# Optimization experiments

Hardware: AMD Instinct MI355X
Metric: run time of the kernel (lower is better)

Reference implementation:

```python
import jax, jax.numpy as jnp
import numpy as np

EPS = 1e-10
WS = 5  # window_size
PAD = WS // 2


def _conv(x, k, pad_h, pad_w):
    # x: [N,1,H,W], k: [1,1,kh,kw], 'same'-style explicit padding
    return jax.lax.conv_general_dilated(
        x, k, window_strides=(1, 1),
        padding=[(pad_h, pad_h), (pad_w, pad_w)],
        dimension_numbers=("NCHW", "OIHW", "NCHW"))


def setup_inputs() -> dict:
    key = jax.random.key(0)
    B, C, Fr, T = 8, 2, 256, 2048
    spectrogram = jax.random.normal(key, (B, C, Fr, T), dtype=jnp.float32)
    # Gaussian kernel (window_size=5, sigma=1.0)
    c = WS // 2
    coords = jnp.arange(WS, dtype=jnp.float32) - c
    yy, xx = jnp.meshgrid(coords, coords, indexing="ij")
    g = jnp.exp(-(xx ** 2 + yy ** 2) / 2.0)
    gaussian_kernel = (g / g.sum()).reshape(1, 1, WS, WS)
    # Sobel kernels / 8
    sobel_x = (jnp.array([[-1, 0, 1], [-2, 0, 2], [-1, 0, 1]], jnp.float32) / 8.0).reshape(1, 1, 3, 3)
    sobel_y = (jnp.array([[-1, -2, -1], [0, 0, 0], [1, 2, 1]], jnp.float32) / 8.0).reshape(1, 1, 3, 3)
    # Harmonic kernel: 7x1 [-1,0,0,2,0,0,-1]
    hk = jnp.zeros(7, jnp.float32).at[0].set(-1.0).at[3].set(2.0).at[6].set(-1.0)
    harmonic_kernel = hk.reshape(1, 1, 7, 1)
    return {"spectrogram": spectrogram, "gaussian_kernel": gaussian_kernel,
            "sobel_x": sobel_x, "sobel_y": sobel_y, "harmonic_kernel": harmonic_kernel}


def _forward(spectrogram, gaussian_kernel, sobel_x, sobel_y, harmonic_kernel):
    B, C, Fr, T = spectrogram.shape
    # Per-channel 1-in/1-out convs == fold channels into batch.
    x = spectrogram.reshape(B * C, 1, Fr, T)

    grad_freq = _conv(x, sobel_y, 1, 1)
    grad_time = _conv(x, sobel_x, 1, 1)
    magnitude = jnp.sqrt(grad_freq ** 2 + grad_time ** 2 + EPS)
    angle = jnp.arctan2(grad_freq, grad_time + EPS)

    # ---- entropy (structure-tensor eigenvalue entropy) ----
    vx = magnitude * jnp.cos(angle)
    vy = magnitude * jnp.sin(angle)
    vxx = _conv(vx * vx, gaussian_kernel, PAD, PAD)
    vyy = _conv(vy * vy, gaussian_kernel, PAD, PAD)
    vxy = _conv(vx * vy, gaussian_kernel, PAD, PAD)
    trace = vxx + vyy
    det = vxx * vyy - vxy * vxy
    disc = jnp.sqrt(jnp.maximum(trace * trace - 4.0 * det, 0.0) + EPS)
    l1 = jnp.maximum((trace + disc) / 2.0, EPS)
    l2 = jnp.maximum((trace - disc) / 2.0, EPS)
    s = l1 + l2 + EPS
    p1, p2 = l1 / s, l2 / s
    entropy = -(p1 * jnp.log(p1 + EPS) + p2 * jnp.log(p2 + EPS)) / np.log(2.0)
    entropy = jnp.clip(entropy, 0.0, 1.0)

    # ---- alignment ----
    ux = jnp.cos(angle)
    uy = jnp.sin(angle)
    ux_avg = _conv(ux, gaussian_kernel, PAD, PAD)
    uy_avg = _conv(uy, gaussian_kernel, PAD, PAD)
    alignment = jnp.clip(jnp.sqrt(ux_avg ** 2 + uy_avg ** 2 + EPS), 0.0, 1.0)

    # ---- curvature ----
    dudx = _conv(ux, sobel_x, 1, 1)
    dudy = _conv(ux, sobel_y, 1, 1)
    dvdx = _conv(uy, sobel_x, 1, 1)
    dvdy = _conv(uy, sobel_y, 1, 1)
    curv = jnp.sqrt(dudx ** 2 + dudy ** 2 + dvdx ** 2 + dvdy ** 2 + EPS)
    curvature = _conv(curv, gaussian_kernel, PAD, PAD)

    # ---- harmonic coherence ----
    harm = jnp.abs(_conv(x, harmonic_kernel, 3, 0))
    local_energy = _conv(x ** 2, gaussian_kernel, PAD, PAD)
    harmonic = jnp.clip(harm / (local_energy + EPS), 0.0, 1.0)

    # ---- temporal stability: inverse temporal gradient magnitude, smoothed ----
    temporal = _conv(1.0 / (1.0 + jnp.abs(grad_time)), gaussian_kernel, PAD, PAD)
    temporal = jnp.clip(temporal, 0.0, 1.0)

    # ---- spectral flow: smoothed frequency-gradient magnitude ----
    spectral = jnp.clip(_conv(jnp.abs(grad_freq), gaussian_kernel, PAD, PAD), 0.0, 1.0)

    def chan_mean(f):  # [B*C,1,F,T] -> [B,1,F,T]
        return f.reshape(B, C, Fr, T).mean(axis=1, keepdims=True)

    return (chan_mean(entropy), chan_mean(alignment), chan_mean(curvature),
            chan_mean(harmonic), chan_mean(temporal), chan_mean(spectral))


def reference(spectrogram, gaussian_kernel, sobel_x, sobel_y, harmonic_kernel):
    return _forward(spectrogram, gaussian_kernel, sobel_x, sobel_y, harmonic_kernel)
```

## Files before the change

kernel.cpp:

```cpp
#include <hip/hip_runtime.h>
#include <hip/hip_fp16.h>


#define F_DIM 256
#define T_DIM 2048
#define B_DIM 8
#define C_DIM 2
#define TILE  32

#define XROWS 40
#define XS    42
#define UROWS 38
#define US    38
#define FROWS 36
#define FS    36
#define FH2   18
#define EPSF  1e-10f

static __device__ __forceinline__ __half2 pack_h2(float a, float b) {
    auto v = __builtin_amdgcn_cvt_pkrtz(a, b);
    return *(__half2*)&v;
}
static __device__ __forceinline__ float clamp01(float x) {
    return fminf(fmaxf(x, 0.f), 1.f);
}

__global__ __launch_bounds__(256, 4)
void audio_struct_fused(const float* __restrict__ x_in,
                        const float* __restrict__ gk_in,
                        float* __restrict__ out)
{
    __shared__ __align__(16) float   s_x [XROWS*XS];
    __shared__ __align__(16) __half2 s_u [UROWS*US];
    __shared__ __align__(16) __half2 s_P0[FROWS*FS];
    __shared__ __align__(16) __half2 s_P1[FROWS*FS];
    __shared__ __align__(16) __half2 s_P2[FROWS*FS];
    __shared__ __align__(16) float   s_tmp[TILE*FS];

    const int tx  = threadIdx.x;
    const int ty  = threadIdx.y;
    const int tid = ty * 32 + tx;
    const int t0  = blockIdx.x * TILE;
    const int f0  = blockIdx.y * TILE;
    const int b   = blockIdx.z;

    float r0 = gk_in[10], r1 = gk_in[11], r2 = gk_in[12], r3 = gk_in[13], r4 = gk_in[14];
    float winv = __builtin_amdgcn_rcpf(r0 + r1 + r2 + r3 + r4);
    const float w[5] = {r0*winv, r1*winv, r2*winv, r3*winv, r4*winv};
    const __half2 wh2[5] = {pack_h2(w[0],w[0]), pack_h2(w[1],w[1]), pack_h2(w[2],w[2]),
                            pack_h2(w[3],w[3]), pack_h2(w[4],w[4])};

    auto vpass_pair = [&](const __half2* src, __half2* dst) {
        const uint2* s = (const uint2*)src;
        uint2* d = (uint2*)dst;
        for (int idx = tid; idx < TILE * FH2; idx += 256) {
            __half2 a0 = pack_h2(0.f, 0.f), a1 = a0;
            #pragma unroll
            for (int i = 0; i < 5; ++i) {
                uint2 v = s[idx + i * FH2];
                a0 = __hfma2(wh2[i], *(const __half2*)&v.x, a0);
                a1 = __hfma2(wh2[i], *(const __half2*)&v.y, a1);
            }
            uint2 o; o.x = *(const unsigned*)&a0; o.y = *(const unsigned*)&a1;
            d[idx] = o;
        }
    };

    float acc[6][4];
    #pragma unroll
    for (int k = 0; k < 6; ++k)
        #pragma unroll
        for (int s = 0; s < 4; ++s) acc[k][s] = 0.0f;

    for (int c = 0; c < C_DIM; ++c) {
        __syncthreads();

        const float* xp = x_in + (size_t)(b * C_DIM + c) * F_DIM * T_DIM;
        for (int idx = tid; idx < XROWS * 20; idx += 256) {
            int r  = idx / 20, c2 = idx % 20;
            int gf = f0 + r - 4;
            int gt = t0 + c2 * 2 - 4;
            float2 v = make_float2(0.f, 0.f);
            if ((unsigned)gf < (unsigned)F_DIM && (unsigned)gt < (unsigned)T_DIM)
                v = *(const float2*)(xp + (size_t)gf * T_DIM + gt);
            *(float2*)&s_x[r * XS + c2 * 2] = v;
        }
        __syncthreads();

        for (int idx = tid; idx < UROWS * UROWS; idx += 256) {
            int r = idx / UROWS, cc = idx % UROWS;
            int gfr = f0 + r - 3, gtc = t0 + cc - 3;
            float ux = 0.f, uy = 0.f, trp = 0.f, dfp = 0.f, sxy = 0.f,
                  tin = 0.f, sf = 0.f;
            if ((unsigned)gfr < (unsigned)F_DIM && (unsigned)gtc < (unsigned)T_DIM) {
                const float* xc = &s_x[(r + 1) * XS + (cc + 1)];
                float x00 = xc[-XS-1], x01 = xc[-XS], x02 = xc[-XS+1];
                float x10 = xc[-1],                   x12 = xc[1];
                float x20 = xc[XS-1],  x21 = xc[XS],  x22 = xc[XS+1];
                float gfv = ((x20 + 2.f*x21 + x22) - (x00 + 2.f*x01 + x02)) * 0.125f;
                float gtv = ((x02 + 2.f*x12 + x22) - (x00 + 2.f*x10 + x20)) * 0.125f;
                float gte = gtv + EPSF;
                float rh  = __builtin_amdgcn_rsqf(gfv * gfv + gte * gte);
                ux = gte * rh;
                uy = gfv * rh;
                float mag = __builtin_amdgcn_sqrtf(gfv * gfv + gtv * gtv + EPSF);
                float vx = mag * ux, vy = mag * uy;
                trp = vx * vx + vy * vy;
                dfp = (vx - vy) * (vx + vy);
                sxy = vx * vy;
                tin = __builtin_amdgcn_rcpf(1.0f + fabsf(gtv));
                sf  = fabsf(gfv);
            }
            s_u[r * US + cc] = pack_h2(ux, uy);
            if (r >= 1 && r < UROWS - 1 && cc >= 1 && cc < UROWS - 1) {
                int fi = (r - 1) * FS + (cc - 1);
                s_P0[fi] = pack_h2(trp, dfp);
                s_P1[fi] = pack_h2(sxy, tin);
                s_P2[fi] = pack_h2(sf, 0.f);
            }
        }
        __syncthreads();

        for (int idx = tid; idx < FROWS * FROWS; idx += 256) {
            int r = idx / FROWS, cc = idx % FROWS;
            int gfr = f0 + r - 2, gtc = t0 + cc - 2;
            float cv = 0.0f;
            if ((unsigned)gfr < (unsigned)F_DIM && (unsigned)gtc < (unsigned)T_DIM) {
                const __half2* up = &s_u[r * US + cc];
                float2 u00 = __half22float2(up[0]),      u01 = __half22float2(up[1]),       u02 = __half22float2(up[2]);
                float2 u10 = __half22float2(up[US]),                                        u12 = __half22float2(up[US+2]);
                float2 u20 = __half22float2(up[2*US]),   u21 = __half22float2(up[2*US+1]),  u22 = __half22float2(up[2*US+2]);
                float dudx = ((u02.x + 2.f*u12.x + u22.x) - (u00.x + 2.f*u10.x + u20.x)) * 0.125f;
                float dudy = ((u20.x + 2.f*u21.x + u22.x) - (u00.x + 2.f*u01.x + u02.x)) * 0.125f;
                float dvdx = ((u02.y + 2.f*u12.y + u22.y) - (u00.y + 2.f*u10.y + u20.y)) * 0.125f;
                float dvdy = ((u20.y + 2.f*u21.y + u22.y) - (u00.y + 2.f*u01.y + u02.y)) * 0.125f;
                cv = __builtin_amdgcn_sqrtf(dudx*dudx + dudy*dudy + dvdx*dvdx + dvdy*dvdy + EPSF);
            }
            ((__half*)s_P2)[2 * (r * FS + cc) + 1] = __float2half_rn(cv);
        }
        __syncthreads();

        float trace_s[4], diff_s[4];
        __half2* tmp_h2 = (__half2*)s_tmp;

        vpass_pair(s_P0, tmp_h2);
        __syncthreads();

        #pragma unroll
        for (int s = 0; s < 4; ++s) {
            int ry = ty + 8 * s;
            float a = 0.f, bv = 0.f;
            #pragma unroll
            for (int j = 0; j < 5; ++j) {
                float2 v = __half22float2(tmp_h2[ry * FS + tx + j]);
                a += w[j] * v.x; bv += w[j] * v.y;
            }
            trace_s[s] = a; diff_s[s] = bv;
        }
        vpass_pair(s_P1, s_P0);
        __syncthreads();

        #pragma unroll
        for (int s = 0; s < 4; ++s) {
            int ry = ty + 8 * s;
            __half2 a = pack_h2(0.f, 0.f);
            #pragma unroll
            for (int j = 0; j < 5; ++j)
                a = __hfma2(wh2[j], s_P0[ry * FS + tx + j], a);
            float2 v = __half22float2(a);
            float trace = trace_s[s], diff = diff_s[s];
            float disc  = __builtin_amdgcn_sqrtf(
                              fmaxf(diff * diff + 4.f * v.x * v.x, 0.f) + EPSF);
            float l1 = fmaxf(0.5f * (trace + disc), EPSF);
            float l2 = fmaxf(0.5f * (trace - disc), EPSF);
            float inv = __builtin_amdgcn_rcpf(l1 + l2 + EPSF);
            float p1 = l1 * inv, p2 = l2 * inv;
            float ent = -(p1 * __builtin_amdgcn_logf(p1 + EPSF)
                        + p2 * __builtin_amdgcn_logf(p2 + EPSF));
            acc[0][s] += 0.5f * clamp01(ent);
            acc[4][s] += 0.5f * clamp01(v.y);
        }
        vpass_pair(s_P2, tmp_h2);
        __syncthreads();

        #pragma unroll
        for (int s = 0; s < 4; ++s) {
            int ry = ty + 8 * s;
            __half2 a = pack_h2(0.f, 0.f);
            #pragma unroll
            for (int j = 0; j < 5; ++j)
                a = __hfma2(wh2[j], tmp_h2[ry * FS + tx + j], a);
            float2 v = __half22float2(a);
            acc[5][s] += 0.5f * clamp01(v.x);
            acc[2][s] += 0.5f * v.y;
        }
        for (int idx = tid; idx < TILE * FS; idx += 256) {
            int r = idx / FS, cc = idx % FS;
            __half2 a = pack_h2(0.f, 0.f);
            #pragma unroll
            for (int i = 0; i < 5; ++i)
                a = __hfma2(wh2[i], s_u[(r + i + 1) * US + (cc + 1)], a);
            s_P1[idx] = a;
        }
        __syncthreads();

        #pragma unroll
        for (int s = 0; s < 4; ++s) {
            int ry = ty + 8 * s;
            __half2 a = pack_h2(0.f, 0.f);
            #pragma unroll
            for (int j = 0; j < 5; ++j)
                a = __hfma2(wh2[j], s_P1[ry * FS + tx + j], a);
            float2 v = __half22float2(a);
            acc[1][s] += 0.5f * clamp01(
                __builtin_amdgcn_sqrtf(v.x * v.x + v.y * v.y + EPSF));
        }
        for (int idx = tid; idx < TILE * FS; idx += 256) {
            int r = idx / FS, cc = idx % FS;
            float a = 0.f;
            #pragma unroll
            for (int i = 0; i < 5; ++i) {
                float xv = s_x[(r + i + 2) * XS + (cc + 2)];
                a += w[i] * xv * xv;
            }
            s_tmp[idx] = a;
        }
        __syncthreads();

        #pragma unroll
        for (int s = 0; s < 4; ++s) {
            int ry = ty + 8 * s;
            float le = 0.f;
            #pragma unroll
            for (int j = 0; j < 5; ++j)
                le += w[j] * s_tmp[ry * FS + tx + j];
            float xm  = s_x[(ry + 1) * XS + tx + 4];
            float x0v = s_x[(ry + 4) * XS + tx + 4];
            float xpv = s_x[(ry + 7) * XS + tx + 4];
            float harm = fabsf(2.f * x0v - xm - xpv);
            acc[3][s] += 0.5f * clamp01(harm * __builtin_amdgcn_rcpf(le + EPSF));
        }
    }

    const size_t plane = (size_t)B_DIM * F_DIM * T_DIM;
    const size_t base  = (size_t)b * F_DIM * T_DIM + (size_t)f0 * T_DIM + t0 + tx;
    #pragma unroll
    for (int k = 0; k < 6; ++k)
        #pragma unroll
        for (int s = 0; s < 4; ++s)
            out[k * plane + base + (size_t)(ty + 8 * s) * T_DIM] = acc[k][s];
}

extern "C" void kernel_launch(void* const* d_in, const int* in_sizes, int n_in,
                              void* d_out, int out_size, void* d_ws, size_t ws_size,
                              hipStream_t stream) {
    const float* x  = (const float*)d_in[0];
    const float* gk = (const float*)d_in[1];
    float* out = (float*)d_out;
    dim3 grid(T_DIM / TILE, F_DIM / TILE, B_DIM);
    dim3 block(32, 8);
    audio_struct_fused<<<grid, block, 0, stream>>>(x, gk, out);
}
```

Before: 225.2 us.

## Use persistent blocks with atomic tile queue and register prefetch of next input

Replaces the one-block-per-tile grid with a fixed set of persistent blocks that take tiles from a global atomic counter. Each block prefetches the next channel's or next tile's input halo into registers while computing the current one, so global loads overlap with compute. It also merges a few LDS phases to drop some barriers, computes the curvature Sobel in packed half2, and reuses buffers. The costs are a second small launch to zero the counter, more register pressure from the prefetch buffer, and some lost fp32 precision in curvature.

```diff
diff --git a/kernel.cpp b/kernel.cpp
--- a/kernel.cpp
+++ b/kernel.cpp
@@ -17,6 +17,9 @@
 #define FH2   18
 #define EPSF  1e-10f
 
+#define NT_TILES (B_DIM * (F_DIM/TILE) * (T_DIM/TILE))
+#define NBLOCKS  1280
+
 static __device__ __forceinline__ __half2 pack_h2(float a, float b) {
     auto v = __builtin_amdgcn_cvt_pkrtz(a, b);
     return *(__half2*)&v;
@@ -25,10 +28,13 @@
     return fminf(fmaxf(x, 0.f), 1.f);
 }
 
+__global__ void zero_counter(int* p) { *p = 0; }
+
 __global__ __launch_bounds__(256, 4)
 void audio_struct_fused(const float* __restrict__ x_in,
                         const float* __restrict__ gk_in,
-                        float* __restrict__ out)
+                        float* __restrict__ out,
+                        int* __restrict__ counter)
 {
     __shared__ __align__(16) float   s_x [XROWS*XS];
     __shared__ __align__(16) __half2 s_u [UROWS*US];
@@ -36,19 +42,36 @@
     __shared__ __align__(16) __half2 s_P1[FROWS*FS];
     __shared__ __align__(16) __half2 s_P2[FROWS*FS];
     __shared__ __align__(16) float   s_tmp[TILE*FS];
+    __shared__ int s_next;
 
     const int tx  = threadIdx.x;
     const int ty  = threadIdx.y;
     const int tid = ty * 32 + tx;
-    const int t0  = blockIdx.x * TILE;
-    const int f0  = blockIdx.y * TILE;
-    const int b   = blockIdx.z;
 
     float r0 = gk_in[10], r1 = gk_in[11], r2 = gk_in[12], r3 = gk_in[13], r4 = gk_in[14];
     float winv = __builtin_amdgcn_rcpf(r0 + r1 + r2 + r3 + r4);
     const float w[5] = {r0*winv, r1*winv, r2*winv, r3*winv, r4*winv};
     const __half2 wh2[5] = {pack_h2(w[0],w[0]), pack_h2(w[1],w[1]), pack_h2(w[2],w[2]),
                             pack_h2(w[3],w[3]), pack_h2(w[4],w[4])};
+    const __half2 two_h2 = pack_h2(2.f, 2.f);
+
+    auto prefetch = [&](int tl, int c, float2* pre) {
+        int bb = tl >> 9, rm = tl & 511;
+        int ff0 = (rm >> 6) << 5, tt0 = (rm & 63) << 5;
+        const float* xp = x_in + (size_t)(bb * C_DIM + c) * F_DIM * T_DIM;
+        bool ok = (tl < NT_TILES);
+        #pragma unroll
+        for (int k = 0; k < 4; ++k) {
+            int idx = tid + 256 * k;
+            int r = idx / 20, c2 = idx % 20;
+            int gf = ff0 + r - 4, gt = tt0 + c2 * 2 - 4;
+            float2 v = make_float2(0.f, 0.f);
+            if (ok && idx < 800 &&
+                (unsigned)gf < (unsigned)F_DIM && (unsigned)gt < (unsigned)T_DIM)
+                v = *(const float2*)(xp + (size_t)gf * T_DIM + gt);
+            pre[k] = v;
+        }
+    };
 
     auto vpass_pair = [&](const __half2* src, __half2* dst) {
         const uint2* s = (const uint2*)src;
@@ -66,189 +89,213 @@
         }
     };
 
-    float acc[6][4];
-    #pragma unroll
-    for (int k = 0; k < 6; ++k)
+    if (tid == 0) s_next = atomicAdd(counter, 1);
+    __syncthreads();
+    int tile = s_next;
+    float2 pre[4];
+    prefetch(tile, 0, pre);
+
+    while (tile < NT_TILES) {
+        const int b   = tile >> 9;
+        const int rem = tile & 511;
+        const int f0  = (rem >> 6) << 5;
+        const int t0  = (rem & 63) << 5;
+        int tile_next = tile;
+
+        float acc[6][4];
         #pragma unroll
-        for (int s = 0; s < 4; ++s) acc[k][s] = 0.0f;
-
-    for (int c = 0; c < C_DIM; ++c) {
-        __syncthreads();
-
-        const float* xp = x_in + (size_t)(b * C_DIM + c) * F_DIM * T_DIM;
-        for (int idx = tid; idx < XROWS * 20; idx += 256) {
-            int r  = idx / 20, c2 = idx % 20;
-            int gf = f0 + r - 4;
-            int gt = t0 + c2 * 2 - 4;
-            float2 v = make_float2(0.f, 0.f);
-            if ((unsigned)gf < (unsigned)F_DIM && (unsigned)gt < (unsigned)T_DIM)
-                v = *(const float2*)(xp + (size_t)gf * T_DIM + gt);
-            *(float2*)&s_x[r * XS + c2 * 2] = v;
+        for (int k = 0; k < 6; ++k)
+            #pragma unroll
+            for (int s = 0; s < 4; ++s) acc[k][s] = 0.0f;
+
+        for (int c = 0; c < C_DIM; ++c) {
+            __syncthreads();
+
+            #pragma unroll
+            for (int k = 0; k < 4; ++k) {
+                int idx = tid + 256 * k;
+                if (idx < 800) {
+                    int r = idx / 20, c2 = idx % 20;
+                    *(float2*)&s_x[r * XS + c2 * 2] = pre[k];
+                }
+            }
+            if (c == 0) {
+                prefetch(tile, 1, pre);
+            } else if (tid == 0) {
+                s_next = atomicAdd(counter, 1);
+            }
+            __syncthreads();
+            if (c == 1) {
+                tile_next = s_next;
+                prefetch(tile_next, 0, pre);
+            }
+
+            for (int idx = tid; idx < UROWS * UROWS; idx += 256) {
+                int r = idx / UROWS, cc = idx % UROWS;
+                int gfr = f0 + r - 3, gtc = t0 + cc - 3;
+                float ux = 0.f, uy = 0.f, trp = 0.f, dfp = 0.f, sxy = 0.f,
+                      tin = 0.f, sf = 0.f;
+                if ((unsigned)gfr < (unsigned)F_DIM && (unsigned)gtc < (unsigned)T_DIM) {
+                    const float* xc = &s_x[(r + 1) * XS + (cc + 1)];
+                    float x00 = xc[-XS-1], x01 = xc[-XS], x02 = xc[-XS+1];
+                    float x10 = xc[-1],                   x12 = xc[1];
+                    float x20 = xc[XS-1],  x21 = xc[XS],  x22 = xc[XS+1];
+                    float gfv = ((x20 + 2.f*x21 + x22) - (x00 + 2.f*x01 + x02)) * 0.125f;
+                    float gtv = ((x02 + 2.f*x12 + x22) - (x00 + 2.f*x10 + x20)) * 0.125f;
+                    float gte = gtv + EPSF;
+                    float rh  = __builtin_amdgcn_rsqf(gfv * gfv + gte * gte);
+                    ux = gte * rh;
+                    uy = gfv * rh;
+                    float mag = __builtin_amdgcn_sqrtf(gfv * gfv + gtv * gtv + EPSF);
+                    float vx = mag * ux, vy = mag * uy;
+                    trp = vx * vx + vy * vy;
+                    dfp = (vx - vy) * (vx + vy);
+                    sxy = vx * vy;
+                    tin = __builtin_amdgcn_rcpf(1.0f + fabsf(gtv));
+                    sf  = fabsf(gfv);
+                }
+                s_u[r * US + cc] = pack_h2(ux, uy);
+                if (r >= 1 && r < UROWS - 1 && cc >= 1 && cc < UROWS - 1) {
+                    int fi = (r - 1) * FS + (cc - 1);
+                    s_P0[fi] = pack_h2(trp, dfp);
+                    s_P1[fi] = pack_h2(sxy, tin);
+                    s_P2[fi] = pack_h2(sf, 0.f);
+                }
+            }
+            __syncthreads();
+
+            __half2* tmp_h2 = (__half2*)s_tmp;
+            for (int idx = tid; idx < FROWS * FROWS; idx += 256) {
+                int r = idx / FROWS, cc = idx % FROWS;
+                int gfr = f0 + r - 2, gtc = t0 + cc - 2;
+                float cv = 0.0f;
+                if ((unsigned)gfr < (unsigned)F_DIM && (unsigned)gtc < (unsigned)T_DIM) {
+                    const __half2* up = &s_u[r * US + cc];
+                    __half2 u00 = up[0],      u01 = up[1],       u02 = up[2];
+                    __half2 u10 = up[US],                        u12 = up[US+2];
+                    __half2 u20 = up[2*US],   u21 = up[2*US+1],  u22 = up[2*US+2];
+                    __half2 vs0 = __hfma2(two_h2, u10, __hadd2(u00, u20));
+                    __half2 vs2 = __hfma2(two_h2, u12, __hadd2(u02, u22));
+                    __half2 hs0 = __hfma2(two_h2, u01, __hadd2(u00, u02));
+                    __half2 hs2 = __hfma2(two_h2, u21, __hadd2(u20, u22));
+                    __half2 dx  = __hsub2(vs2, vs0);
+                    __half2 dy  = __hsub2(hs2, hs0);
+                    __half2 sq  = __hfma2(dy, dy, __hmul2(dx, dx));
+                    float ssum = __low2float(sq) + __high2float(sq);
+                    cv = __builtin_amdgcn_sqrtf(ssum * 0.015625f + EPSF);
+                }
+                ((__half*)s_P2)[2 * (r * FS + cc) + 1] = __float2half_rn(cv);
+            }
+            vpass_pair(s_P0, tmp_h2);
+            __syncthreads();
+
+            float trace_s[4], diff_s[4];
+            #pragma unroll
+            for (int s = 0; s < 4; ++s) {
+                int ry = ty + 8 * s;
+                float a = 0.f, bv = 0.f;
+                #pragma unroll
+                for (int j = 0; j < 5; ++j) {
+                    float2 v = __half22float2(tmp_h2[ry * FS + tx + j]);
+                    a += w[j] * v.x; bv += w[j] * v.y;
+                }
+                trace_s[s] = a; diff_s[s] = bv;
+            }
+            vpass_pair(s_P1, s_P0);
+            __syncthreads();
+
+            #pragma unroll
+            for (int s = 0; s < 4; ++s) {
+                int ry = ty + 8 * s;
+                __half2 a = pack_h2(0.f, 0.f);
+                #pragma unroll
+                for (int j = 0; j < 5; ++j)
+                    a = __hfma2(wh2[j], s_P0[ry * FS + tx + j], a);
+                float2 v = __half22float2(a);
+                float trace = trace_s[s], diff = diff_s[s];
+                float disc  = __builtin_amdgcn_sqrtf(
+                                  fmaxf(diff * diff + 4.f * v.x * v.x, 0.f) + EPSF);
+                float l1 = fmaxf(0.5f * (trace + disc), EPSF);
+                float l2 = fmaxf(0.5f * (trace - disc), EPSF);
+                float inv = __builtin_amdgcn_rcpf(l1 + l2 + EPSF);
+                float p1 = l1 * inv, p2 = l2 * inv;
+                float ent = -(p1 * __builtin_amdgcn_logf(p1 + EPSF)
+                            + p2 * __builtin_amdgcn_logf(p2 + EPSF));
+                acc[0][s] += 0.5f * clamp01(ent);
+                acc[4][s] += 0.5f * clamp01(v.y);
+            }
+            vpass_pair(s_P2, tmp_h2);
+            for (int idx = tid; idx < TILE * FS; idx += 256) {
+                int r = idx / FS, cc = idx % FS;
+                __half2 a = pack_h2(0.f, 0.f);
+                #pragma unroll
+                for (int i = 0; i < 5; ++i)
+                    a = __hfma2(wh2[i], s_u[(r + i + 1) * US + (cc + 1)], a);
+                s_P1[idx] = a;
+            }
+            __syncthreads();
+
+            #pragma unroll
+            for (int s = 0; s < 4; ++s) {
+                int ry = ty + 8 * s;
+                __half2 a = pack_h2(0.f, 0.f);
+                #pragma unroll
+                for (int j = 0; j < 5; ++j)
+                    a = __hfma2(wh2[j], tmp_h2[ry * FS + tx + j], a);
+                float2 v = __half22float2(a);
+                acc[5][s] += 0.5f * clamp01(v.x);
+                acc[2][s] += 0.5f * v.y;
+                __half2 a2 = pack_h2(0.f, 0.f);
+                #pragma unroll
+                for (int j = 0; j < 5; ++j)
+                    a2 = __hfma2(wh2[j], s_P1[ry * FS + tx + j], a2);
+                float2 u = __half22float2(a2);
+                acc[1][s] += 0.5f * clamp01(
+                    __builtin_amdgcn_sqrtf(u.x * u.x + u.y * u.y + EPSF));
+            }
+            {
+                float* xv2 = (float*)s_P0;
+                for (int idx = tid; idx < TILE * FS; idx += 256) {
+                    int r = idx / FS, cc = idx % FS;
+                    float a = 0.f;
+                    #pragma unroll
+                    for (int i = 0; i < 5; ++i) {
+                        float xv = s_x[(r + i + 2) * XS + (cc + 2)];
+                        a += w[i] * xv * xv;
+                    }
+                    xv2[idx] = a;
+                }
+            }
+            __syncthreads();
+
+            {
+                const float* xv2 = (const float*)s_P0;
+                #pragma unroll
+                for (int s = 0; s < 4; ++s) {
+                    int ry = ty + 8 * s;
+                    float le = 0.f;
+                    #pragma unroll
+                    for (int j = 0; j < 5; ++j)
+                        le += w[j] * xv2[ry * FS + tx + j];
+                    float xm  = s_x[(ry + 1) * XS + tx + 4];
+                    float x0v = s_x[(ry + 4) * XS + tx + 4];
+                    float xpv = s_x[(ry + 7) * XS + tx + 4];
+                    float harm = fabsf(2.f * x0v - xm - xpv);
+                    acc[3][s] += 0.5f * clamp01(harm * __builtin_amdgcn_rcpf(le + EPSF));
+                }
+            }
         }
-        __syncthreads();
-
-        for (int idx = tid; idx < UROWS * UROWS; idx += 256) {
-            int r = idx / UROWS, cc = idx % UROWS;
-            int gfr = f0 + r - 3, gtc = t0 + cc - 3;
-            float ux = 0.f, uy = 0.f, trp = 0.f, dfp = 0.f, sxy = 0.f,
-                  tin = 0.f, sf = 0.f;
-            if ((unsigned)gfr < (unsigned)F_DIM && (unsigned)gtc < (unsigned)T_DIM) {
-                const float* xc = &s_x[(r + 1) * XS + (cc + 1)];
-                float x00 = xc[-XS-1], x01 = xc[-XS], x02 = xc[-XS+1];
-                float x10 = xc[-1],                   x12 = xc[1];
-                float x20 = xc[XS-1],  x21 = xc[XS],  x22 = xc[XS+1];
-                float gfv = ((x20 + 2.f*x21 + x22) - (x00 + 2.f*x01 + x02)) * 0.125f;
-                float gtv = ((x02 + 2.f*x12 + x22) - (x00 + 2.f*x10 + x20)) * 0.125f;
-                float gte = gtv + EPSF;
-                float rh  = __builtin_amdgcn_rsqf(gfv * gfv + gte * gte);
-                ux = gte * rh;
-                uy = gfv * rh;
-                float mag = __builtin_amdgcn_sqrtf(gfv * gfv + gtv * gtv + EPSF);
-                float vx = mag * ux, vy = mag * uy;
-                trp = vx * vx + vy * vy;
-                dfp = (vx - vy) * (vx + vy);
-                sxy = vx * vy;
-                tin = __builtin_amdgcn_rcpf(1.0f + fabsf(gtv));
-                sf  = fabsf(gfv);
-            }
-            s_u[r * US + cc] = pack_h2(ux, uy);
-            if (r >= 1 && r < UROWS - 1 && cc >= 1 && cc < UROWS - 1) {
-                int fi = (r - 1) * FS + (cc - 1);
-                s_P0[fi] = pack_h2(trp, dfp);
-                s_P1[fi] = pack_h2(sxy, tin);
-                s_P2[fi] = pack_h2(sf, 0.f);
-            }
-        }
-        __syncthreads();
-
-        for (int idx = tid; idx < FROWS * FROWS; idx += 256) {
-            int r = idx / FROWS, cc = idx % FROWS;
-            int gfr = f0 + r - 2, gtc = t0 + cc - 2;
-            float cv = 0.0f;
-            if ((unsigned)gfr < (unsigned)F_DIM && (unsigned)gtc < (unsigned)T_DIM) {
-                const __half2* up = &s_u[r * US + cc];
-                float2 u00 = __half22float2(up[0]),      u01 = __half22float2(up[1]),       u02 = __half22float2(up[2]);
-                float2 u10 = __half22float2(up[US]),                                        u12 = __half22float2(up[US+2]);
-                float2 u20 = __half22float2(up[2*US]),   u21 = __half22float2(up[2*US+1]),  u22 = __half22float2(up[2*US+2]);
-                float dudx = ((u02.x + 2.f*u12.x + u22.x) - (u00.x + 2.f*u10.x + u20.x)) * 0.125f;
-                float dudy = ((u20.x + 2.f*u21.x + u22.x) - (u00.x + 2.f*u01.x + u02.x)) * 0.125f;
-                float dvdx = ((u02.y + 2.f*u12.y + u22.y) - (u00.y + 2.f*u10.y + u20.y)) * 0.125f;
-                float dvdy = ((u20.y + 2.f*u21.y + u22.y) - (u00.y + 2.f*u01.y + u02.y)) * 0.125f;
-                cv = __builtin_amdgcn_sqrtf(dudx*dudx + dudy*dudy + dvdx*dvdx + dvdy*dvdy + EPSF);
-            }
-            ((__half*)s_P2)[2 * (r * FS + cc) + 1] = __float2half_rn(cv);
-        }
-        __syncthreads();
-
-        float trace_s[4], diff_s[4];
-        __half2* tmp_h2 = (__half2*)s_tmp;
-
-        vpass_pair(s_P0, tmp_h2);
-        __syncthreads();
-
+
+        const size_t plane = (size_t)B_DIM * F_DIM * T_DIM;
+        const size_t base  = (size_t)b * F_DIM * T_DIM + (size_t)f0 * T_DIM + t0 + tx;
         #pragma unroll
-        for (int s = 0; s < 4; ++s) {
-            int ry = ty + 8 * s;
-            float a = 0.f, bv = 0.f;
-            #pragma unroll
-            for (int j = 0; j < 5; ++j) {
-                float2 v = __half22float2(tmp_h2[ry * FS + tx + j]);
-                a += w[j] * v.x; bv += w[j] * v.y;
-            }
-            trace_s[s] = a; diff_s[s] = bv;
-        }
-        vpass_pair(s_P1, s_P0);
-        __syncthreads();
-
-        #pragma unroll
-        for (int s = 0; s < 4; ++s) {
-            int ry = ty + 8 * s;
-            __half2 a = pack_h2(0.f, 0.f);
-            #pragma unroll
-            for (int j = 0; j < 5; ++j)
-                a = __hfma2(wh2[j], s_P0[ry * FS + tx + j], a);
-            float2 v = __half22float2(a);
-            float trace = trace_s[s], diff = diff_s[s];
-            float disc  = __builtin_amdgcn_sqrtf(
-                              fmaxf(diff * diff + 4.f * v.x * v.x, 0.f) + EPSF);
-            float l1 = fmaxf(0.5f * (trace + disc), EPSF);
-            float l2 = fmaxf(0.5f * (trace - disc), EPSF);
-            float inv = __builtin_amdgcn_rcpf(l1 + l2 + EPSF);
-            float p1 = l1 * inv, p2 = l2 * inv;
-            float ent = -(p1 * __builtin_amdgcn_logf(p1 + EPSF)
-                        + p2 * __builtin_amdgcn_logf(p2 + EPSF));
-            acc[0][s] += 0.5f * clamp01(ent);
-            acc[4][s] += 0.5f * clamp01(v.y);
-        }
-        vpass_pair(s_P2, tmp_h2);
-        __syncthreads();
-
-        #pragma unroll
-        for (int s = 0; s < 4; ++s) {
-            int ry = ty + 8 * s;
-            __half2 a = pack_h2(0.f, 0.f);
-            #pragma unroll
-            for (int j = 0; j < 5; ++j)
-                a = __hfma2(wh2[j], tmp_h2[ry * FS + tx + j], a);
-            float2 v = __half22float2(a);
-            acc[5][s] += 0.5f * clamp01(v.x);
-            acc[2][s] += 0.5f * v.y;
-        }
-        for (int idx = tid; idx < TILE * FS; idx += 256) {
-            int r = idx / FS, cc = idx % FS;
-            __half2 a = pack_h2(0.f, 0.f);
-            #pragma unroll
-            for (int i = 0; i < 5; ++i)
-                a = __hfma2(wh2[i], s_u[(r + i + 1) * US + (cc + 1)], a);
-            s_P1[idx] = a;
-        }
-        __syncthreads();
-
-        #pragma unroll
-        for (int s = 0; s < 4; ++s) {
-            int ry = ty + 8 * s;
-            __half2 a = pack_h2(0.f, 0.f);
-            #pragma unroll
-            for (int j = 0; j < 5; ++j)
-                a = __hfma2(wh2[j], s_P1[ry * FS + tx + j], a);
-            float2 v = __half22float2(a);
-            acc[1][s] += 0.5f * clamp01(
-                __builtin_amdgcn_sqrtf(v.x * v.x + v.y * v.y + EPSF));
-        }
-        for (int idx = tid; idx < TILE * FS; idx += 256) {
-            int r = idx / FS, cc = idx % FS;
-            float a = 0.f;
-            #pragma unroll
-            for (int i = 0; i < 5; ++i) {
-                float xv = s_x[(r + i + 2) * XS + (cc + 2)];
-                a += w[i] * xv * xv;
-            }
-            s_tmp[idx] = a;
-        }
-        __syncthreads();
-
-        #pragma unroll
-        for (int s = 0; s < 4; ++s) {
-            int ry = ty + 8 * s;
-            float le = 0.f;
-            #pragma unroll
-            for (int j = 0; j < 5; ++j)
-                le += w[j] * s_tmp[ry * FS + tx + j];
-            float xm  = s_x[(ry + 1) * XS + tx + 4];
-            float x0v = s_x[(ry + 4) * XS + tx + 4];
-            float xpv = s_x[(ry + 7) * XS + tx + 4];
-            float harm = fabsf(2.f * x0v - xm - xpv);
-            acc[3][s] += 0.5f * clamp01(harm * __builtin_amdgcn_rcpf(le + EPSF));
-        }
+        for (int k = 0; k < 6; ++k)
+            #pragma unroll
+            for (int s = 0; s < 4; ++s)
+                out[k * plane + base + (size_t)(ty + 8 * s) * T_DIM] = acc[k][s];
+
+        tile = tile_next;
     }
-
-    const size_t plane = (size_t)B_DIM * F_DIM * T_DIM;
-    const size_t base  = (size_t)b * F_DIM * T_DIM + (size_t)f0 * T_DIM + t0 + tx;
-    #pragma unroll
-    for (int k = 0; k < 6; ++k)
-        #pragma unroll
-        for (int s = 0; s < 4; ++s)
-            out[k * plane + base + (size_t)(ty + 8 * s) * T_DIM] = acc[k][s];
 }
 
 extern "C" void kernel_launch(void* const* d_in, const int* in_sizes, int n_in,
@@ -257,7 +304,8 @@
     const float* x  = (const float*)d_in[0];
     const float* gk = (const float*)d_in[1];
     float* out = (float*)d_out;
-    dim3 grid(T_DIM / TILE, F_DIM / TILE, B_DIM);
+    int* counter = (int*)d_ws;
+    zero_counter<<<1, 1, 0, stream>>>(counter);
     dim3 block(32, 8);
-    audio_struct_fused<<<grid, block, 0, stream>>>(x, gk, out);
+    audio_struct_fused<<<NBLOCKS, block, 0, stream>>>(x, gk, out, counter);
 }
```

After: 278.6 us. 1.24x slower.
